# Kernel optimization log

Measured on AMD Instinct MI355X. Metric: run time of the kernel, lower is better.

The kernel has to match this reference:

```python
import jax, jax.numpy as jnp
import numpy as np

B, L, K, D_IN, UNITS, LATENT = 4, 4096, 32, 128, 128, 64


def setup_inputs() -> dict:
    key = jax.random.key(0)
    ks = jax.random.split(key, 8)
    s = 1.0 / np.sqrt(D_IN)
    return {
        "x": jax.random.normal(ks[0], (B, L, D_IN), jnp.float32),
        "position_embedding": jax.random.normal(ks[1], (B, L, K, UNITS), jnp.float32),
        "nn_idx": jax.random.randint(ks[2], (B, L, K), 0, L, jnp.int32),
        "Wq": jax.random.normal(ks[3], (D_IN, UNITS), jnp.float32) * s,
        "Wk": jax.random.normal(ks[4], (D_IN, UNITS), jnp.float32) * s,
        "Wv": jax.random.normal(ks[5], (D_IN, UNITS), jnp.float32) * s,
        "Wa0": jax.random.normal(ks[6], (UNITS, LATENT), jnp.float32) * (1.0 / np.sqrt(UNITS)),
        "Wa1": jax.random.normal(ks[7], (LATENT, UNITS), jnp.float32) * (1.0 / np.sqrt(LATENT)),
    }


def reference(x, position_embedding, nn_idx, Wq, Wk, Wv, Wa0, Wa1):
    # projections: [B,L,units]
    query = x @ Wq
    key = x @ Wk
    value = x @ Wv

    # per-batch gather of K neighbors along the length axis -> [B,L,K,units]
    gather = jax.vmap(lambda t, idx: t[idx])
    key_n = gather(key, nn_idx)
    val_n = gather(value, nn_idx)

    # relative query-key relation: [B,L,K,units]
    qk = query[:, :, None, :] - key_n

    # position-aware attention MLP: relu(Dense) -> Dense, softmax over neighbor axis K
    attn = jax.nn.relu((qk + position_embedding) @ Wa0) @ Wa1
    attn = jax.nn.softmax(attn, axis=-2)  # per-channel softmax over K

    # weighted aggregation over neighbors -> [B,L,units]
    out = jnp.sum((val_n + position_embedding) * attn, axis=-2)
    return out
```

## Files before the change

### kernel.cpp

```cpp
#include <hip/hip_runtime.h>

#define BL 16384
#define LQ 4096
#define VPS 136

typedef unsigned int uint;
typedef unsigned short ushort;
typedef __attribute__((ext_vector_type(8))) short short8;
typedef __attribute__((ext_vector_type(4))) float floatx4;

union F8 { uint u[4]; uint4 u4; short8 s; };

static __device__ __forceinline__ uint f2bf(float f) {
    uint x = __float_as_uint(f);
    x += 0x7fffu + ((x >> 16) & 1u);
    return x >> 16;
}
static __device__ __forceinline__ float bf2f(uint h) { return __uint_as_float(h << 16); }
static __device__ __forceinline__ uint pk(float lo, float hi) {
    return f2bf(lo) | (f2bf(hi) << 16);
}

__global__ __launch_bounds__(256, 4) void qkv_mfma(
    const float* __restrict__ x, const float* __restrict__ Wq,
    const float* __restrict__ Wk, const float* __restrict__ Wv,
    float* __restrict__ qkvb)
{
    __shared__ uint4 wfh[4][8][64];
    __shared__ uint4 wfl[4][8][64];
    const int tid  = threadIdx.x;
    const int lane = tid & 63;
    const int w    = tid >> 6;
    const int q    = lane >> 4;
    const int c    = lane & 15;
    const int proj = blockIdx.y;
    const float* W = (proj == 0) ? Wq : (proj == 1) ? Wk : Wv;
    float* outb = qkvb + (size_t)proj * BL * 128;

    for (int e = tid; e < 32 * 64; e += 256) {
        const int f = e >> 6, ln = e & 63;
        const int ks = f >> 3, Nt = f & 7;
        const int lq = ln >> 4, lc = ln & 15;
        const float* wp = W + (ks * 32 + lq * 8) * 128 + Nt * 16 + lc;
        F8 hi, lo;
        #pragma unroll
        for (int j = 0; j < 4; ++j) {
            const float a = wp[(2 * j) * 128], b = wp[(2 * j + 1) * 128];
            const uint ha = f2bf(a), hb = f2bf(b);
            hi.u[j] = ha | (hb << 16);
            lo.u[j] = pk(a - bf2f(ha), b - bf2f(hb));
        }
        wfh[ks][Nt][ln] = hi.u4;
        wfl[ks][Nt][ln] = lo.u4;
    }
    __syncthreads();

    floatx4 acc[8];
    #pragma unroll
    for (int i = 0; i < 8; ++i) acc[i] = {0.f, 0.f, 0.f, 0.f};

    const int arow = blockIdx.x * 64 + w * 16 + c;
    #pragma unroll
    for (int ks = 0; ks < 4; ++ks) {
        const float* xp = x + arow * 128 + ks * 32 + q * 8;
        const float4 xa = ((const float4*)xp)[0];
        const float4 xb = ((const float4*)xp)[1];
        const float xv[8] = {xa.x, xa.y, xa.z, xa.w, xb.x, xb.y, xb.z, xb.w};
        F8 xh, xl;
        #pragma unroll
        for (int j = 0; j < 4; ++j) {
            const uint ha = f2bf(xv[2 * j]), hb = f2bf(xv[2 * j + 1]);
            xh.u[j] = ha | (hb << 16);
            xl.u[j] = pk(xv[2 * j] - bf2f(ha), xv[2 * j + 1] - bf2f(hb));
        }
        #pragma unroll
        for (int Nt = 0; Nt < 8; ++Nt) {
            F8 wh, wl;
            wh.u4 = wfh[ks][Nt][lane];
            wl.u4 = wfl[ks][Nt][lane];
            acc[Nt] = __builtin_amdgcn_mfma_f32_16x16x32_bf16(xh.s, wh.s, acc[Nt], 0, 0, 0);
            acc[Nt] = __builtin_amdgcn_mfma_f32_16x16x32_bf16(xh.s, wl.s, acc[Nt], 0, 0, 0);
            acc[Nt] = __builtin_amdgcn_mfma_f32_16x16x32_bf16(xl.s, wh.s, acc[Nt], 0, 0, 0);
        }
    }
    const int orow = blockIdx.x * 64 + w * 16 + q * 4;
    #pragma unroll
    for (int Nt = 0; Nt < 8; ++Nt)
        #pragma unroll
        for (int r = 0; r < 4; ++r)
            outb[(orow + r) * 128 + Nt * 16 + c] = acc[Nt][r];
}

__global__ __launch_bounds__(256, 2) void attn_mfma(
    const float* __restrict__ pos, const int* __restrict__ nn_idx,
    const float* __restrict__ qb, const float* __restrict__ kb,
    const float* __restrict__ vb, const float* __restrict__ Wa0,
    const float* __restrict__ Wa1, float* __restrict__ out)
{
    __shared__ uint4 wa0f[16][64];
    __shared__ uint4 wa1f[16][64];
    __shared__ __attribute__((aligned(16))) ushort vpL[4][32 * VPS];

    const int tid  = threadIdx.x;
    const int lane = tid & 63;
    const int w    = tid >> 6;
    const int q    = lane >> 4;
    const int c    = lane & 15;

    for (int e = tid; e < 16 * 64; e += 256) {
        const int f = e >> 6, ln = e & 63;
        const int Mt = f >> 2, ks = f & 3;
        const int lq = ln >> 4, lc = ln & 15;
        const float* wp = Wa0 + (ks * 32 + lq * 8) * 64 + Mt * 16 + lc;
        F8 v;
        #pragma unroll
        for (int j = 0; j < 4; ++j) v.u[j] = pk(wp[(2 * j) * 64], wp[(2 * j + 1) * 64]);
        wa0f[f][ln] = v.u4;
    }
    for (int e = tid; e < 16 * 64; e += 256) {
        const int f = e >> 6, ln = e & 63;
        const int ks = f >> 3, Nt = f & 7;
        const int lq = ln >> 4, lc = ln & 15;
        const float* wp = Wa1 + (ks * 32 + lq * 8) * 128 + Nt * 16 + lc;
        F8 v;
        #pragma unroll
        for (int j = 0; j < 4; ++j) v.u[j] = pk(wp[(2 * j) * 128], wp[(2 * j + 1) * 128]);
        wa1f[f][ln] = v.u4;
    }
    __syncthreads();

    const int pbase = (blockIdx.x * 4 + w) * 8;

    float4 PF[4][2][2];
    int pidx0, pidx1;
    {
        const int p = pbase;
        pidx0 = nn_idx[p * 32 + c];
        pidx1 = nn_idx[p * 32 + 16 + c];
        #pragma unroll
        for (int ks = 0; ks < 4; ++ks)
            #pragma unroll
            for (int Nt = 0; Nt < 2; ++Nt) {
                const float* pp = pos + ((size_t)(p * 32 + Nt * 16 + c) * 128 + ks * 32 + q * 8);
                PF[ks][Nt][0] = ((const float4*)pp)[0];
                PF[ks][Nt][1] = ((const float4*)pp)[1];
            }
    }

    for (int it = 0; it < 8; ++it) {
        const int p     = pbase + it;
        const int bbase = (p >> 12) << 12;
        const int r0    = (bbase + pidx0) * 128;
        const int r1    = (bbase + pidx1) * 128;

        float4 qv[4][2];
        #pragma unroll
        for (int ks = 0; ks < 4; ++ks) {
            const float* qp = qb + p * 128 + ks * 32 + q * 8;
            qv[ks][0] = ((const float4*)qp)[0];
            qv[ks][1] = ((const float4*)qp)[1];
        }

        floatx4 acc1[4][2];
        #pragma unroll
        for (int i = 0; i < 4; ++i) { acc1[i][0] = {0.f,0.f,0.f,0.f}; acc1[i][1] = {0.f,0.f,0.f,0.f}; }

        #pragma unroll
        for (int ks = 0; ks < 4; ++ks) {
            const int u0 = ks * 32 + q * 8;
            F8 bfrag[2];
            #pragma unroll
            for (int Nt = 0; Nt < 2; ++Nt) {
                const int kr = (Nt ? r1 : r0) + u0;
                const float4 ka = *(const float4*)(kb + kr);
                const float4 kc = *(const float4*)(kb + kr + 4);
                const float4 va = *(const float4*)(vb + kr);
                const float4 vc = *(const float4*)(vb + kr + 4);
                const float4 pa = PF[ks][Nt][0];
                const float4 pc = PF[ks][Nt][1];
                const float4 qa = qv[ks][0], qc = qv[ks][1];
                const float t0 = qa.x - ka.x + pa.x, t1 = qa.y - ka.y + pa.y;
                const float t2 = qa.z - ka.z + pa.z, t3 = qa.w - ka.w + pa.w;
                const float t4 = qc.x - kc.x + pc.x, t5 = qc.y - kc.y + pc.y;
                const float t6 = qc.z - kc.z + pc.z, t7 = qc.w - kc.w + pc.w;
                bfrag[Nt].u[0] = pk(t0, t1); bfrag[Nt].u[1] = pk(t2, t3);
                bfrag[Nt].u[2] = pk(t4, t5); bfrag[Nt].u[3] = pk(t6, t7);
                F8 vpp;
                vpp.u[0] = pk(va.x + pa.x, va.y + pa.y);
                vpp.u[1] = pk(va.z + pa.z, va.w + pa.w);
                vpp.u[2] = pk(vc.x + pc.x, vc.y + pc.y);
                vpp.u[3] = pk(vc.z + pc.z, vc.w + pc.w);
                *(uint4*)&vpL[w][(Nt * 16 + c) * VPS + u0] = vpp.u4;
            }
            #pragma unroll
            for (int Mt = 0; Mt < 4; ++Mt) {
                F8 a1; a1.u4 = wa0f[Mt * 4 + ks][lane];
                acc1[Mt][0] = __builtin_amdgcn_mfma_f32_16x16x32_bf16(a1.s, bfrag[0].s, acc1[Mt][0], 0, 0, 0);
                acc1[Mt][1] = __builtin_amdgcn_mfma_f32_16x16x32_bf16(a1.s, bfrag[1].s, acc1[Mt][1], 0, 0, 0);
            }
        }

        {
            const int pn = (p + 1 < BL) ? (p + 1) : p;
            pidx0 = nn_idx[pn * 32 + c];
            pidx1 = nn_idx[pn * 32 + 16 + c];
            #pragma unroll
            for (int ks = 0; ks < 4; ++ks)
                #pragma unroll
                for (int Nt = 0; Nt < 2; ++Nt) {
                    const float* pp = pos + ((size_t)(pn * 32 + Nt * 16 + c) * 128 + ks * 32 + q * 8);
                    PF[ks][Nt][0] = ((const float4*)pp)[0];
                    PF[ks][Nt][1] = ((const float4*)pp)[1];
                }
        }

        F8 a2[2][2];
        #pragma unroll
        for (int Mt2 = 0; Mt2 < 2; ++Mt2) {
            #pragma unroll
            for (int ks = 0; ks < 2; ++ks) {
                float vv[8];
                #pragma unroll
                for (int t = 0; t < 8; ++t) {
                    const int sl = c + 16 * ((q & 1) * 2 + (t >> 2));
                    const float vA = __shfl(acc1[2 * ks + 0][Mt2][t & 3], sl, 64);
                    const float vB = __shfl(acc1[2 * ks + 1][Mt2][t & 3], sl, 64);
                    vv[t] = fmaxf((q < 2) ? vA : vB, 0.f);
                }
                #pragma unroll
                for (int j = 0; j < 4; ++j) a2[Mt2][ks].u[j] = pk(vv[2 * j], vv[2 * j + 1]);
            }
        }

        #pragma unroll
        for (int Nt2 = 0; Nt2 < 8; ++Nt2) {
            F8 b0, b1;
            b0.u4 = wa1f[Nt2][lane];
            b1.u4 = wa1f[8 + Nt2][lane];
            floatx4 a2c[2];
            a2c[0] = {0.f,0.f,0.f,0.f}; a2c[1] = {0.f,0.f,0.f,0.f};
            #pragma unroll
            for (int Mt2 = 0; Mt2 < 2; ++Mt2) {
                a2c[Mt2] = __builtin_amdgcn_mfma_f32_16x16x32_bf16(a2[Mt2][0].s, b0.s, a2c[Mt2], 0, 0, 0);
                a2c[Mt2] = __builtin_amdgcn_mfma_f32_16x16x32_bf16(a2[Mt2][1].s, b1.s, a2c[Mt2], 0, 0, 0);
            }
            const int cg = Nt2 * 16 + c;
            float se = 0.f, ov = 0.f;
            #pragma unroll
            for (int Mt2 = 0; Mt2 < 2; ++Mt2)
                #pragma unroll
                for (int r = 0; r < 4; ++r) {
                    const int   kk = Mt2 * 16 + q * 4 + r;
                    const float e  = __expf(a2c[Mt2][r]);
                    const float vp = bf2f(vpL[w][kk * VPS + cg]);
                    se += e;
                    ov = fmaf(e, vp, ov);
                }
            se += __shfl_xor(se, 16, 64); ov += __shfl_xor(ov, 16, 64);
            se += __shfl_xor(se, 32, 64); ov += __shfl_xor(ov, 32, 64);
            if (q == 0) out[p * 128 + cg] = ov / se;
        }
    }
}

extern "C" void kernel_launch(void* const* d_in, const int* in_sizes, int n_in,
                              void* d_out, int out_size, void* d_ws, size_t ws_size,
                              hipStream_t stream) {
    const float* x    = (const float*)d_in[0];
    const float* pos  = (const float*)d_in[1];
    const int*   nidx = (const int*)  d_in[2];
    const float* Wq   = (const float*)d_in[3];
    const float* Wk   = (const float*)d_in[4];
    const float* Wv   = (const float*)d_in[5];
    const float* Wa0  = (const float*)d_in[6];
    const float* Wa1  = (const float*)d_in[7];
    float* outp = (float*)d_out;

    float* qkvb = (float*)d_ws;
    const float* qbp = qkvb;
    const float* kbp = qkvb + (size_t)BL * 128;
    const float* vbp = qkvb + (size_t)2 * BL * 128;

    qkv_mfma<<<dim3(BL / 64, 3), 256, 0, stream>>>(x, Wq, Wk, Wv, qkvb);
    attn_mfma<<<BL / 8 / 4, 256, 0, stream>>>(pos, nidx, qbp, kbp, vbp, Wa0, Wa1, outp);
}
```

Before: 476.9 us.

## Store K/V projections in bf16, fuse QKV projections, prefetch indices and query

```diff
diff --git a/kernel.cpp b/kernel.cpp
--- a/kernel.cpp
+++ b/kernel.cpp
@@ -8,6 +8,8 @@
 typedef unsigned short ushort;
 typedef __attribute__((ext_vector_type(8))) short short8;
 typedef __attribute__((ext_vector_type(4))) float floatx4;
+typedef __attribute__((ext_vector_type(4))) float fv4;
+typedef __attribute__((ext_vector_type(2))) float fv2;
 
 union F8 { uint u[4]; uint4 u4; short8 s; };
 
@@ -17,89 +19,114 @@
     return x >> 16;
 }
 static __device__ __forceinline__ float bf2f(uint h) { return __uint_as_float(h << 16); }
+static __device__ __forceinline__ float bflo(uint p) { return __uint_as_float(p << 16); }
+static __device__ __forceinline__ float bfhi(uint p) { return __uint_as_float(p & 0xffff0000u); }
 static __device__ __forceinline__ uint pk(float lo, float hi) {
     return f2bf(lo) | (f2bf(hi) << 16);
 }
-
-__global__ __launch_bounds__(256, 4) void qkv_mfma(
+static __device__ __forceinline__ fv4 nt4(const float* p) {
+    return __builtin_nontemporal_load((const fv4*)p);
+}
+
+__global__ __launch_bounds__(256, 3) void qkv_mfma(
     const float* __restrict__ x, const float* __restrict__ Wq,
     const float* __restrict__ Wk, const float* __restrict__ Wv,
-    float* __restrict__ qkvb)
+    float* __restrict__ qb, ushort* __restrict__ kb, ushort* __restrict__ vb)
 {
     __shared__ uint4 wfh[4][8][64];
     __shared__ uint4 wfl[4][8][64];
+    __shared__ ushort bb[64 * 128];
     const int tid  = threadIdx.x;
     const int lane = tid & 63;
     const int w    = tid >> 6;
     const int q    = lane >> 4;
     const int c    = lane & 15;
-    const int proj = blockIdx.y;
-    const float* W = (proj == 0) ? Wq : (proj == 1) ? Wk : Wv;
-    float* outb = qkvb + (size_t)proj * BL * 128;
-
-    for (int e = tid; e < 32 * 64; e += 256) {
-        const int f = e >> 6, ln = e & 63;
-        const int ks = f >> 3, Nt = f & 7;
-        const int lq = ln >> 4, lc = ln & 15;
-        const float* wp = W + (ks * 32 + lq * 8) * 128 + Nt * 16 + lc;
-        F8 hi, lo;
-        #pragma unroll
-        for (int j = 0; j < 4; ++j) {
-            const float a = wp[(2 * j) * 128], b = wp[(2 * j + 1) * 128];
-            const uint ha = f2bf(a), hb = f2bf(b);
-            hi.u[j] = ha | (hb << 16);
-            lo.u[j] = pk(a - bf2f(ha), b - bf2f(hb));
-        }
-        wfh[ks][Nt][ln] = hi.u4;
-        wfl[ks][Nt][ln] = lo.u4;
-    }
-    __syncthreads();
-
-    floatx4 acc[8];
-    #pragma unroll
-    for (int i = 0; i < 8; ++i) acc[i] = {0.f, 0.f, 0.f, 0.f};
 
     const int arow = blockIdx.x * 64 + w * 16 + c;
+    F8 xh[4], xl[4];
     #pragma unroll
     for (int ks = 0; ks < 4; ++ks) {
-        const float* xp = x + arow * 128 + ks * 32 + q * 8;
-        const float4 xa = ((const float4*)xp)[0];
-        const float4 xb = ((const float4*)xp)[1];
+        const float* xp = x + (size_t)arow * 128 + ks * 32 + q * 8;
+        const fv4 xa = *(const fv4*)xp;
+        const fv4 xb = *(const fv4*)(xp + 4);
         const float xv[8] = {xa.x, xa.y, xa.z, xa.w, xb.x, xb.y, xb.z, xb.w};
-        F8 xh, xl;
         #pragma unroll
         for (int j = 0; j < 4; ++j) {
             const uint ha = f2bf(xv[2 * j]), hb = f2bf(xv[2 * j + 1]);
-            xh.u[j] = ha | (hb << 16);
-            xl.u[j] = pk(xv[2 * j] - bf2f(ha), xv[2 * j + 1] - bf2f(hb));
-        }
-        #pragma unroll
-        for (int Nt = 0; Nt < 8; ++Nt) {
-            F8 wh, wl;
-            wh.u4 = wfh[ks][Nt][lane];
-            wl.u4 = wfl[ks][Nt][lane];
-            acc[Nt] = __builtin_amdgcn_mfma_f32_16x16x32_bf16(xh.s, wh.s, acc[Nt], 0, 0, 0);
-            acc[Nt] = __builtin_amdgcn_mfma_f32_16x16x32_bf16(xh.s, wl.s, acc[Nt], 0, 0, 0);
-            acc[Nt] = __builtin_amdgcn_mfma_f32_16x16x32_bf16(xl.s, wh.s, acc[Nt], 0, 0, 0);
-        }
-    }
-    const int orow = blockIdx.x * 64 + w * 16 + q * 4;
-    #pragma unroll
-    for (int Nt = 0; Nt < 8; ++Nt)
-        #pragma unroll
-        for (int r = 0; r < 4; ++r)
-            outb[(orow + r) * 128 + Nt * 16 + c] = acc[Nt][r];
+            xh[ks].u[j] = ha | (hb << 16);
+            xl[ks].u[j] = pk(xv[2 * j] - bf2f(ha), xv[2 * j + 1] - bf2f(hb));
+        }
+    }
+
+    for (int proj = 0; proj < 3; ++proj) {
+        const float* W = (proj == 0) ? Wq : (proj == 1) ? Wk : Wv;
+        __syncthreads();
+        for (int e = tid; e < 32 * 64; e += 256) {
+            const int f = e >> 6, ln = e & 63;
+            const int ks = f >> 3, Nt = f & 7;
+            const int lq = ln >> 4, lc = ln & 15;
+            const float* wp = W + (ks * 32 + lq * 8) * 128 + Nt * 16 + lc;
+            F8 hi, lo;
+            #pragma unroll
+            for (int j = 0; j < 4; ++j) {
+                const float a = wp[(2 * j) * 128], b = wp[(2 * j + 1) * 128];
+                const uint ha = f2bf(a), hb = f2bf(b);
+                hi.u[j] = ha | (hb << 16);
+                lo.u[j] = pk(a - bf2f(ha), b - bf2f(hb));
+            }
+            wfh[ks][Nt][ln] = hi.u4;
+            wfl[ks][Nt][ln] = lo.u4;
+        }
+        __syncthreads();
+
+        floatx4 acc[8];
+        #pragma unroll
+        for (int i = 0; i < 8; ++i) acc[i] = {0.f, 0.f, 0.f, 0.f};
+        #pragma unroll
+        for (int ks = 0; ks < 4; ++ks)
+            #pragma unroll
+            for (int Nt = 0; Nt < 8; ++Nt) {
+                F8 wh, wl;
+                wh.u4 = wfh[ks][Nt][lane];
+                wl.u4 = wfl[ks][Nt][lane];
+                acc[Nt] = __builtin_amdgcn_mfma_f32_16x16x32_bf16(xh[ks].s, wh.s, acc[Nt], 0, 0, 0);
+                acc[Nt] = __builtin_amdgcn_mfma_f32_16x16x32_bf16(xh[ks].s, wl.s, acc[Nt], 0, 0, 0);
+                acc[Nt] = __builtin_amdgcn_mfma_f32_16x16x32_bf16(xl[ks].s, wh.s, acc[Nt], 0, 0, 0);
+            }
+
+        if (proj == 0) {
+            const int orow = blockIdx.x * 64 + w * 16 + q * 4;
+            #pragma unroll
+            for (int Nt = 0; Nt < 8; ++Nt)
+                #pragma unroll
+                for (int r = 0; r < 4; ++r)
+                    qb[(size_t)(orow + r) * 128 + Nt * 16 + c] = acc[Nt][r];
+        } else {
+            const int rl = w * 16 + q * 4;
+            #pragma unroll
+            for (int Nt = 0; Nt < 8; ++Nt)
+                #pragma unroll
+                for (int r = 0; r < 4; ++r)
+                    bb[(rl + r) * 128 + Nt * 16 + c] = (ushort)f2bf(acc[Nt][r]);
+            __syncthreads();
+            ushort* kv = (proj == 1) ? kb : vb;
+            uint4* dst = (uint4*)(kv + (size_t)blockIdx.x * 64 * 128);
+            const uint4* src = (const uint4*)bb;
+            for (int e = tid; e < 64 * 128 / 8; e += 256) dst[e] = src[e];
+        }
+    }
 }
 
 __global__ __launch_bounds__(256, 2) void attn_mfma(
     const float* __restrict__ pos, const int* __restrict__ nn_idx,
-    const float* __restrict__ qb, const float* __restrict__ kb,
-    const float* __restrict__ vb, const float* __restrict__ Wa0,
+    const float* __restrict__ qb, const ushort* __restrict__ kb,
+    const ushort* __restrict__ vb, const float* __restrict__ Wa0,
     const float* __restrict__ Wa1, float* __restrict__ out)
 {
     __shared__ uint4 wa0f[16][64];
     __shared__ uint4 wa1f[16][64];
     __shared__ __attribute__((aligned(16))) ushort vpL[4][32 * VPS];
+    __shared__ __attribute__((aligned(16))) float outL[4][128];
 
     const int tid  = threadIdx.x;
     const int lane = tid & 63;
@@ -131,34 +158,44 @@
 
     const int pbase = (blockIdx.x * 4 + w) * 8;
 
-    float4 PF[4][2][2];
-    int pidx0, pidx1;
+    int idx0[8], idx1[8];
+    #pragma unroll
+    for (int it = 0; it < 8; ++it) {
+        idx0[it] = nn_idx[(pbase + it) * 32 + c];
+        idx1[it] = nn_idx[(pbase + it) * 32 + 16 + c];
+    }
+
+    fv4 PF[4][2][2];
+    fv4 PQ[4][2];
     {
         const int p = pbase;
-        pidx0 = nn_idx[p * 32 + c];
-        pidx1 = nn_idx[p * 32 + 16 + c];
-        #pragma unroll
-        for (int ks = 0; ks < 4; ++ks)
+        #pragma unroll
+        for (int ks = 0; ks < 4; ++ks) {
+            PQ[ks][0] = nt4(qb + (size_t)p * 128 + ks * 32 + q * 8);
+            PQ[ks][1] = nt4(qb + (size_t)p * 128 + ks * 32 + q * 8 + 4);
             #pragma unroll
             for (int Nt = 0; Nt < 2; ++Nt) {
                 const float* pp = pos + ((size_t)(p * 32 + Nt * 16 + c) * 128 + ks * 32 + q * 8);
-                PF[ks][Nt][0] = ((const float4*)pp)[0];
-                PF[ks][Nt][1] = ((const float4*)pp)[1];
-            }
+                PF[ks][Nt][0] = nt4(pp);
+                PF[ks][Nt][1] = nt4(pp + 4);
+            }
+        }
     }
 
     for (int it = 0; it < 8; ++it) {
         const int p     = pbase + it;
         const int bbase = (p >> 12) << 12;
-        const int r0    = (bbase + pidx0) * 128;
-        const int r1    = (bbase + pidx1) * 128;
-
-        float4 qv[4][2];
+        const int r0    = (bbase + idx0[it]) * 128;
+        const int r1    = (bbase + idx1[it]) * 128;
+
+        uint4 KR0[4], KR1[4], VR0[4], VR1[4];
         #pragma unroll
         for (int ks = 0; ks < 4; ++ks) {
-            const float* qp = qb + p * 128 + ks * 32 + q * 8;
-            qv[ks][0] = ((const float4*)qp)[0];
-            qv[ks][1] = ((const float4*)qp)[1];
+            const int u0 = ks * 32 + q * 8;
+            KR0[ks] = *(const uint4*)(kb + r0 + u0);
+            KR1[ks] = *(const uint4*)(kb + r1 + u0);
+            VR0[ks] = *(const uint4*)(vb + r0 + u0);
+            VR1[ks] = *(const uint4*)(vb + r1 + u0);
         }
 
         floatx4 acc1[4][2];
@@ -171,25 +208,21 @@
             F8 bfrag[2];
             #pragma unroll
             for (int Nt = 0; Nt < 2; ++Nt) {
-                const int kr = (Nt ? r1 : r0) + u0;
-                const float4 ka = *(const float4*)(kb + kr);
-                const float4 kc = *(const float4*)(kb + kr + 4);
-                const float4 va = *(const float4*)(vb + kr);
-                const float4 vc = *(const float4*)(vb + kr + 4);
-                const float4 pa = PF[ks][Nt][0];
-                const float4 pc = PF[ks][Nt][1];
-                const float4 qa = qv[ks][0], qc = qv[ks][1];
-                const float t0 = qa.x - ka.x + pa.x, t1 = qa.y - ka.y + pa.y;
-                const float t2 = qa.z - ka.z + pa.z, t3 = qa.w - ka.w + pa.w;
-                const float t4 = qc.x - kc.x + pc.x, t5 = qc.y - kc.y + pc.y;
-                const float t6 = qc.z - kc.z + pc.z, t7 = qc.w - kc.w + pc.w;
+                const uint4 ku = Nt ? KR1[ks] : KR0[ks];
+                const uint4 vu = Nt ? VR1[ks] : VR0[ks];
+                const fv4 pa = PF[ks][Nt][0], pc = PF[ks][Nt][1];
+                const fv4 qa = PQ[ks][0],    qc = PQ[ks][1];
+                const float t0 = qa.x - bflo(ku.x) + pa.x, t1 = qa.y - bfhi(ku.x) + pa.y;
+                const float t2 = qa.z - bflo(ku.y) + pa.z, t3 = qa.w - bfhi(ku.y) + pa.w;
+                const float t4 = qc.x - bflo(ku.z) + pc.x, t5 = qc.y - bfhi(ku.z) + pc.y;
+                const float t6 = qc.z - bflo(ku.w) + pc.z, t7 = qc.w - bfhi(ku.w) + pc.w;
                 bfrag[Nt].u[0] = pk(t0, t1); bfrag[Nt].u[1] = pk(t2, t3);
                 bfrag[Nt].u[2] = pk(t4, t5); bfrag[Nt].u[3] = pk(t6, t7);
                 F8 vpp;
-                vpp.u[0] = pk(va.x + pa.x, va.y + pa.y);
-                vpp.u[1] = pk(va.z + pa.z, va.w + pa.w);
-                vpp.u[2] = pk(vc.x + pc.x, vc.y + pc.y);
-                vpp.u[3] = pk(vc.z + pc.z, vc.w + pc.w);
+                vpp.u[0] = pk(bflo(vu.x) + pa.x, bfhi(vu.x) + pa.y);
+                vpp.u[1] = pk(bflo(vu.y) + pa.z, bfhi(vu.y) + pa.w);
+                vpp.u[2] = pk(bflo(vu.z) + pc.x, bfhi(vu.z) + pc.y);
+                vpp.u[3] = pk(bflo(vu.w) + pc.z, bfhi(vu.w) + pc.w);
                 *(uint4*)&vpL[w][(Nt * 16 + c) * VPS + u0] = vpp.u4;
             }
             #pragma unroll
@@ -202,16 +235,17 @@
 
         {
             const int pn = (p + 1 < BL) ? (p + 1) : p;
-            pidx0 = nn_idx[pn * 32 + c];
-            pidx1 = nn_idx[pn * 32 + 16 + c];
-            #pragma unroll
-            for (int ks = 0; ks < 4; ++ks)
+            #pragma unroll
+            for (int ks = 0; ks < 4; ++ks) {
+                PQ[ks][0] = nt4(qb + (size_t)pn * 128 + ks * 32 + q * 8);
+                PQ[ks][1] = nt4(qb + (size_t)pn * 128 + ks * 32 + q * 8 + 4);
                 #pragma unroll
                 for (int Nt = 0; Nt < 2; ++Nt) {
                     const float* pp = pos + ((size_t)(pn * 32 + Nt * 16 + c) * 128 + ks * 32 + q * 8);
-                    PF[ks][Nt][0] = ((const float4*)pp)[0];
-                    PF[ks][Nt][1] = ((const float4*)pp)[1];
+                    PF[ks][Nt][0] = nt4(pp);
+                    PF[ks][Nt][1] = nt4(pp + 4);
                 }
+            }
         }
 
         F8 a2[2][2];
@@ -258,7 +292,11 @@
                 }
             se += __shfl_xor(se, 16, 64); ov += __shfl_xor(ov, 16, 64);
             se += __shfl_xor(se, 32, 64); ov += __shfl_xor(ov, 32, 64);
-            if (q == 0) out[p * 128 + cg] = ov / se;
+            if (q == 0) outL[w][cg] = ov / se;
+        }
+        {
+            const fv2 o2 = *(const fv2*)&outL[w][lane * 2];
+            __builtin_nontemporal_store(o2, (fv2*)(out + (size_t)p * 128 + lane * 2));
         }
     }
 }
@@ -276,11 +314,10 @@
     const float* Wa1  = (const float*)d_in[7];
     float* outp = (float*)d_out;
 
-    float* qkvb = (float*)d_ws;
-    const float* qbp = qkvb;
-    const float* kbp = qkvb + (size_t)BL * 128;
-    const float* vbp = qkvb + (size_t)2 * BL * 128;
-
-    qkv_mfma<<<dim3(BL / 64, 3), 256, 0, stream>>>(x, Wq, Wk, Wv, qkvb);
+    float*  qbp = (float*)d_ws;
+    ushort* kbp = (ushort*)((char*)d_ws + (size_t)BL * 128 * 4);
+    ushort* vbp = kbp + (size_t)BL * 128;
+
+    qkv_mfma<<<BL / 64, 256, 0, stream>>>(x, Wq, Wk, Wv, qbp, kbp, vbp);
     attn_mfma<<<BL / 8 / 4, 256, 0, stream>>>(pos, nidx, qbp, kbp, vbp, Wa0, Wa1, outp);
 }
```

Result: slower. 569.5 us (+19.4%).
